# Kernel optimization log

Measured on AMD Instinct MI355X. Metric: run time of the kernel, lower is better.

## Reference

```python
import jax, jax.numpy as jnp
import numpy as np

B, C, M, N = 16, 512, 256, 4096

def setup_inputs() -> dict:
    key = jax.random.key(0)
    k1, k2, k3 = jax.random.split(key, 3)
    x = jax.random.normal(k1, (B, C, N), dtype=jnp.float32)
    # Conv1d(C, M, 1, bias=False) weight: [M, C] (kernel size 1 squeezed)
    Wk = jax.random.normal(k2, (M, C), dtype=jnp.float32) * (1.0 / np.sqrt(C))
    # Conv1d(M, C, 1, bias=False) weight: [C, M]
    Wv = jax.random.normal(k3, (C, M), dtype=jnp.float32) * (1.0 / np.sqrt(M))
    return {"x": x, "Wk": Wk, "Wv": Wv}

def reference(x, Wk, Wv):
    # attn = M_k(x): 1x1 conv == matmul over channel dim -> [B, M, N]
    attn = jnp.einsum("mc,bcn->bmn", Wk, x)
    # softmax over sequence dim N
    attn = jax.nn.softmax(attn, axis=2)
    # L1 normalization over memory-unit (channel) dim M
    attn = attn / (1e-9 + attn.sum(axis=1, keepdims=True))
    # out = M_v(attn): [B, C, N]
    out = jnp.einsum("cm,bmn->bcn", Wv, attn)
    return x + out
```

## Files before the change

kernel.cpp:

```cpp
#include <hip/hip_runtime.h>
#include <hip/hip_bf16.h>

#define Bdim 16
#define Cdim 512
#define Mdim 256
#define Ndim 4096

typedef short bf16x8 __attribute__((ext_vector_type(8)));
typedef float f32x4 __attribute__((ext_vector_type(4)));
typedef unsigned short us8 __attribute__((ext_vector_type(8)));
typedef unsigned short us4 __attribute__((ext_vector_type(4)));

__device__ __forceinline__ unsigned short f2b(float f) {
  union { float f; unsigned int u; } v; v.f = f;
  return (unsigned short)((v.u + 0x8000u) >> 16);
}
__device__ __forceinline__ float b2f(unsigned short h) {
  union { unsigned int u; float f; } v; v.u = ((unsigned int)h) << 16;
  return v.f;
}

__global__ __launch_bounds__(256) void k0_convert(
    const float* __restrict__ gWk, const float* __restrict__ gWv,
    unsigned short* __restrict__ oWk, unsigned short* __restrict__ oWv) {
  const int i = (blockIdx.x * 256 + threadIdx.x) * 4;
  f32x4 a = *reinterpret_cast<const f32x4*>(gWk + i);
  f32x4 b = *reinterpret_cast<const f32x4*>(gWv + i);
  us4 ha, hb;
#pragma unroll
  for (int j = 0; j < 4; ++j) { ha[j] = f2b(a[j]); hb[j] = f2b(b[j]); }
  *reinterpret_cast<us4*>(oWk + i) = ha;
  *reinterpret_cast<us4*>(oWv + i) = hb;
}

#define K1_XPAD 72

__global__ __launch_bounds__(256) void k1_gemm1(
    const float* __restrict__ gx, const unsigned short* __restrict__ gWkB,
    unsigned short* __restrict__ gS) {
  __shared__ unsigned short Wk_s[128 * 64];
  __shared__ unsigned short xT_s[128 * K1_XPAD];
  const int t = threadIdx.x;
  const int b = blockIdx.z;
  const int m0 = blockIdx.y * 128;
  const int n0 = blockIdx.x * 128;
  const int w = t >> 6;
  const int lane = t & 63;
  const int lr = lane & 15;
  const int lg = lane >> 4;
  const int wm = (w >> 1) * 64;
  const int wn = (w & 1) * 64;

  f32x4 acc[4][4] = {};
  const float* xb = gx + (size_t)b * Cdim * Ndim + n0;

  const int snl = t & 63;
  const int scb = (t >> 6) * 16;

  for (int ck = 0; ck < Cdim; ck += 64) {
    {
      const unsigned short* gsrc =
          gWkB + (size_t)(m0 + w * 32 + (lane >> 3)) * Cdim + ck + (lane & 7) * 8;
#pragma unroll
      for (int j = 0; j < 4; ++j) {
        __builtin_amdgcn_global_load_lds(
            (const __attribute__((address_space(1))) unsigned int*)(gsrc + (size_t)j * 8 * Cdim),
            (__attribute__((address_space(3))) unsigned int*)&Wk_s[(w * 32 + j * 8) * 64],
            16, 0, 0);
      }
    }
#pragma unroll
    for (int h = 0; h < 2; ++h) {
      const int n = snl + h * 64;
      const float* src = xb + (size_t)(ck + scb) * Ndim + n;
      float xv[16];
#pragma unroll
      for (int j = 0; j < 16; ++j) xv[j] = src[(size_t)j * Ndim];
      us8 h0, h1;
#pragma unroll
      for (int j = 0; j < 8; ++j) {
        h0[j] = (unsigned short)(__float_as_uint(xv[j]) >> 16);
        h1[j] = (unsigned short)(__float_as_uint(xv[8 + j]) >> 16);
      }
      *reinterpret_cast<us8*>(&xT_s[n * K1_XPAD + scb]) = h0;
      *reinterpret_cast<us8*>(&xT_s[n * K1_XPAD + scb + 8]) = h1;
    }
    __syncthreads();
#pragma unroll
    for (int kk = 0; kk < 64; kk += 32) {
      bf16x8 af[4], bfr[4];
#pragma unroll
      for (int mi = 0; mi < 4; ++mi)
        af[mi] = *reinterpret_cast<const bf16x8*>(
            &Wk_s[(wm + mi * 16 + lr) * 64 + kk + lg * 8]);
#pragma unroll
      for (int ni = 0; ni < 4; ++ni)
        bfr[ni] = *reinterpret_cast<const bf16x8*>(
            &xT_s[(wn + ni * 16 + lr) * K1_XPAD + kk + lg * 8]);
#pragma unroll
      for (int mi = 0; mi < 4; ++mi)
#pragma unroll
        for (int ni = 0; ni < 4; ++ni)
          acc[mi][ni] = __builtin_amdgcn_mfma_f32_16x16x32_bf16(
              af[mi], bfr[ni], acc[mi][ni], 0, 0, 0);
    }
    __syncthreads();
  }
  unsigned short* Sb = gS + ((size_t)b * Mdim + m0 + wm) * Ndim + n0 + wn;
#pragma unroll
  for (int mi = 0; mi < 4; ++mi)
#pragma unroll
    for (int ni = 0; ni < 4; ++ni)
#pragma unroll
      for (int r = 0; r < 4; ++r) {
        int m = mi * 16 + lg * 4 + r;
        int n = ni * 16 + lr;
        Sb[(size_t)m * Ndim + n] = f2b(acc[mi][ni][r]);
      }
}

__global__ __launch_bounds__(256) void k2_rowstats(
    const unsigned short* __restrict__ gS, float2* __restrict__ stats) {
  const int m = blockIdx.x;
  const int b = blockIdx.y;
  const unsigned short* row = gS + ((size_t)b * Mdim + m) * Ndim;
  const int t = threadIdx.x;
  const int w = t >> 6;
  float v[16];
#pragma unroll
  for (int i = 0; i < 2; ++i) {
    us8 u = *reinterpret_cast<const us8*>(row + i * 2048 + t * 8);
#pragma unroll
    for (int j = 0; j < 8; ++j) v[i * 8 + j] = b2f(u[j]);
  }
  float mx = -1e30f;
#pragma unroll
  for (int i = 0; i < 16; ++i) mx = fmaxf(mx, v[i]);
#pragma unroll
  for (int o = 32; o > 0; o >>= 1) mx = fmaxf(mx, __shfl_xor(mx, o, 64));
  __shared__ float redmax[4], redsum[4];
  if ((t & 63) == 0) redmax[w] = mx;
  __syncthreads();
  mx = fmaxf(fmaxf(redmax[0], redmax[1]), fmaxf(redmax[2], redmax[3]));
  float s = 0.f;
#pragma unroll
  for (int i = 0; i < 16; ++i) s += __expf(v[i] - mx);
#pragma unroll
  for (int o = 32; o > 0; o >>= 1) s += __shfl_xor(s, o, 64);
  if ((t & 63) == 0) redsum[w] = s;
  __syncthreads();
  if (t == 0) {
    float tot = redsum[0] + redsum[1] + redsum[2] + redsum[3];
    stats[(size_t)b * Mdim + m] = make_float2(mx, 1.0f / tot);
  }
}

#define K3_PAD 264

__global__ __launch_bounds__(256) void k3_norm(
    const unsigned short* __restrict__ gS, const float2* __restrict__ stats,
    unsigned short* __restrict__ gPT) {
  __shared__ unsigned short P_s[64 * K3_PAD];
  __shared__ float cs[4][64];
  __shared__ float rtot[64];
  const int b = blockIdx.y;
  const int n0 = blockIdx.x * 64;
  const int t = threadIdx.x;
  const int w = t >> 6;
  const int l = t & 63;
  const unsigned short* Sb = gS + ((size_t)b * Mdim + w * 64) * Ndim + n0 + l;
  const float2* stb = stats + (size_t)b * Mdim + w * 64;
  float acc = 0.f;
#pragma unroll
  for (int i8 = 0; i8 < 8; ++i8) {
    us8 pk;
#pragma unroll
    for (int jj = 0; jj < 8; ++jj) {
      const int mi = i8 * 8 + jj;
      float2 st = stb[mi];
      float p = __expf(b2f(Sb[(size_t)mi * Ndim]) - st.x) * st.y;
      acc += p;
      pk[jj] = f2b(p);
    }
    *reinterpret_cast<us8*>(&P_s[l * K3_PAD + w * 64 + i8 * 8]) = pk;
  }
  cs[w][l] = acc;
  __syncthreads();
  if (w == 0) rtot[l] = 1.0f / (1e-9f + cs[0][l] + cs[1][l] + cs[2][l] + cs[3][l]);
  __syncthreads();
  const int mo = (t & 31) * 8;
#pragma unroll
  for (int j = 0; j < 8; ++j) {
    const int n = (t >> 5) + j * 8;
    const float rc = rtot[n];
    us8 pv = *reinterpret_cast<const us8*>(&P_s[n * K3_PAD + mo]);
    us8 o;
#pragma unroll
    for (int q = 0; q < 8; ++q) o[q] = f2b(b2f(pv[q]) * rc);
    *reinterpret_cast<us8*>(gPT + ((size_t)b * Ndim + n0 + n) * Mdim + mo) = o;
  }
}

__global__ __launch_bounds__(256) void k4_gemm2(
    const float* __restrict__ gx, const unsigned short* __restrict__ gWvB,
    const unsigned short* __restrict__ gPT, float* __restrict__ gout) {
  __shared__ unsigned short PT_s[2][128 * 128];
  const int t = threadIdx.x;
  const int b = blockIdx.z;
  const int c0 = blockIdx.y * 128;
  const int n0 = blockIdx.x * 128;
  const int w = t >> 6;
  const int lane = t & 63;
  const int lr = lane & 15;
  const int lg = lane >> 4;
  const int wc = (w >> 1) * 64;
  const int wn = (w & 1) * 64;

  f32x4 acc[4][4] = {};

  {
    const int mo16 = (t & 15) * 16;
    const int r0 = t >> 4;
#pragma unroll
    for (int s = 0; s < 2; ++s) {
      char* tile = reinterpret_cast<char*>(PT_s[s]);
#pragma unroll
      for (int j = 0; j < 8; ++j) {
        const int n = r0 + j * 16;
        us8 v = *reinterpret_cast<const us8*>(
            reinterpret_cast<const char*>(gPT) +
            ((size_t)b * Ndim + n0 + n) * (Mdim * 2) + s * 256 + mo16);
        *reinterpret_cast<us8*>(tile + n * 256 + (mo16 ^ ((n & 7) << 4))) = v;
      }
    }
  }
  __syncthreads();
#pragma unroll
  for (int s = 0; s < 2; ++s) {
    const unsigned short* WvRow = gWvB + (size_t)(c0 + wc + lr) * Mdim + s * 128 + lg * 8;
    const char* tile = reinterpret_cast<const char*>(PT_s[s]);
#pragma unroll
    for (int kk = 0; kk < 128; kk += 32) {
      bf16x8 af[4], bfr[4];
#pragma unroll
      for (int ci = 0; ci < 4; ++ci)
        af[ci] = *reinterpret_cast<const bf16x8*>(WvRow + (size_t)ci * 16 * Mdim + kk);
#pragma unroll
      for (int ni = 0; ni < 4; ++ni) {
        const int rn = wn + ni * 16 + lr;
        bfr[ni] = *reinterpret_cast<const bf16x8*>(
            tile + ((rn * 256 + (kk + lg * 8) * 2) ^ ((rn & 7) << 4)));
      }
#pragma unroll
      for (int ci = 0; ci < 4; ++ci)
#pragma unroll
        for (int ni = 0; ni < 4; ++ni)
          acc[ci][ni] = __builtin_amdgcn_mfma_f32_16x16x32_bf16(
              af[ci], bfr[ni], acc[ci][ni], 0, 0, 0);
    }
  }
  const size_t base = ((size_t)b * Cdim + c0 + wc) * Ndim + n0 + wn;
#pragma unroll
  for (int ci = 0; ci < 4; ++ci)
#pragma unroll
    for (int ni = 0; ni < 4; ++ni)
#pragma unroll
      for (int r = 0; r < 4; ++r) {
        size_t idx = base + (size_t)(ci * 16 + lg * 4 + r) * Ndim + ni * 16 + lr;
        gout[idx] = gx[idx] + acc[ci][ni][r];
      }
}

extern "C" void kernel_launch(void* const* d_in, const int* in_sizes, int n_in,
                              void* d_out, int out_size, void* d_ws, size_t ws_size,
                              hipStream_t stream) {
  const float* x = (const float*)d_in[0];
  const float* Wk = (const float*)d_in[1];
  const float* Wv = (const float*)d_in[2];
  float* out = (float*)d_out;

  unsigned short* S = (unsigned short*)d_ws;
  unsigned short* PT = S + (size_t)Bdim * Mdim * Ndim;
  float2* stats = (float2*)(PT + (size_t)Bdim * Ndim * Mdim);
  unsigned short* WkB = (unsigned short*)(stats + Bdim * Mdim);
  unsigned short* WvB = WkB + Mdim * Cdim;

  k0_convert<<<dim3((Mdim * Cdim) / 1024), 256, 0, stream>>>(Wk, Wv, WkB, WvB);
  k1_gemm1<<<dim3(Ndim / 128, Mdim / 128, Bdim), 256, 0, stream>>>(x, WkB, S);
  k2_rowstats<<<dim3(Mdim, Bdim), 256, 0, stream>>>(S, stats);
  k3_norm<<<dim3(Ndim / 64, Bdim), 256, 0, stream>>>(S, stats, PT);
  k4_gemm2<<<dim3(Ndim / 128, Cdim / 128, Bdim), 256, 0, stream>>>(x, WvB, PT, out);
}
```

Baseline: 143.0 us.

## Swizzle Wk LDS tile and stage Wv/PT via direct global-to-LDS loads

In the first GEMM, the Wk tile loaded into LDS is XOR-swizzled by row so the MFMA fragment reads avoid LDS bank conflicts. In the second GEMM, Wv was previously read straight from global memory for every fragment. It is now staged into LDS together with the PT tile using global_load_lds, with matching swizzles, and processed in two K-halves separated by barriers. This removes repeated uncached-pattern global reads and register round-trips, but adds extra synchronisation and less overlap, since each half must land before compute starts.

```diff
diff --git a/kernel.cpp b/kernel.cpp
--- a/kernel.cpp
+++ b/kernel.cpp
@@ -56,11 +56,13 @@
 
   const int snl = t & 63;
   const int scb = (t >> 6) * 16;
+  const int wrow = lane >> 3;
+  const int wchk = (lane & 7) ^ (wrow & 7);
 
   for (int ck = 0; ck < Cdim; ck += 64) {
     {
       const unsigned short* gsrc =
-          gWkB + (size_t)(m0 + w * 32 + (lane >> 3)) * Cdim + ck + (lane & 7) * 8;
+          gWkB + (size_t)(m0 + w * 32 + wrow) * Cdim + ck + wchk * 8;
 #pragma unroll
       for (int j = 0; j < 4; ++j) {
         __builtin_amdgcn_global_load_lds(
@@ -90,9 +92,12 @@
     for (int kk = 0; kk < 64; kk += 32) {
       bf16x8 af[4], bfr[4];
 #pragma unroll
-      for (int mi = 0; mi < 4; ++mi)
+      for (int mi = 0; mi < 4; ++mi) {
+        const int rm = wm + mi * 16 + lr;
         af[mi] = *reinterpret_cast<const bf16x8*>(
-            &Wk_s[(wm + mi * 16 + lr) * 64 + kk + lg * 8]);
+            reinterpret_cast<const char*>(Wk_s) +
+            rm * 128 + ((kk * 2 + lg * 16) ^ ((rm & 7) << 4)));
+      }
 #pragma unroll
       for (int ni = 0; ni < 4; ++ni)
         bfr[ni] = *reinterpret_cast<const bf16x8*>(
@@ -204,7 +209,8 @@
 __global__ __launch_bounds__(256) void k4_gemm2(
     const float* __restrict__ gx, const unsigned short* __restrict__ gWvB,
     const unsigned short* __restrict__ gPT, float* __restrict__ gout) {
-  __shared__ unsigned short PT_s[2][128 * 128];
+  __shared__ unsigned short Wv_s[128 * 128];
+  __shared__ unsigned short PT_s[128 * 128];
   const int t = threadIdx.x;
   const int b = blockIdx.z;
   const int c0 = blockIdx.y * 128;
@@ -218,38 +224,41 @@
 
   f32x4 acc[4][4] = {};
 
-  {
-    const int mo16 = (t & 15) * 16;
-    const int r0 = t >> 4;
-#pragma unroll
-    for (int s = 0; s < 2; ++s) {
-      char* tile = reinterpret_cast<char*>(PT_s[s]);
-#pragma unroll
-      for (int j = 0; j < 8; ++j) {
-        const int n = r0 + j * 16;
-        us8 v = *reinterpret_cast<const us8*>(
-            reinterpret_cast<const char*>(gPT) +
-            ((size_t)b * Ndim + n0 + n) * (Mdim * 2) + s * 256 + mo16);
-        *reinterpret_cast<us8*>(tile + n * 256 + (mo16 ^ ((n & 7) << 4))) = v;
-      }
-    }
-  }
-  __syncthreads();
-#pragma unroll
+  const int srow = lane >> 4;
+
   for (int s = 0; s < 2; ++s) {
-    const unsigned short* WvRow = gWvB + (size_t)(c0 + wc + lr) * Mdim + s * 128 + lg * 8;
-    const char* tile = reinterpret_cast<const char*>(PT_s[s]);
+#pragma unroll
+    for (int j = 0; j < 8; ++j) {
+      const int r = w * 32 + j * 4 + srow;
+      const int chk = (lane & 15) ^ (r & 7);
+      __builtin_amdgcn_global_load_lds(
+          (const __attribute__((address_space(1))) unsigned int*)(
+              gWvB + (size_t)(c0 + r) * Mdim + s * 128 + chk * 8),
+          (__attribute__((address_space(3))) unsigned int*)&Wv_s[(w * 32 + j * 4) * 128],
+          16, 0, 0);
+      __builtin_amdgcn_global_load_lds(
+          (const __attribute__((address_space(1))) unsigned int*)(
+              gPT + ((size_t)b * Ndim + n0 + r) * Mdim + s * 128 + chk * 8),
+          (__attribute__((address_space(3))) unsigned int*)&PT_s[(w * 32 + j * 4) * 128],
+          16, 0, 0);
+    }
+    __syncthreads();
 #pragma unroll
     for (int kk = 0; kk < 128; kk += 32) {
       bf16x8 af[4], bfr[4];
 #pragma unroll
-      for (int ci = 0; ci < 4; ++ci)
-        af[ci] = *reinterpret_cast<const bf16x8*>(WvRow + (size_t)ci * 16 * Mdim + kk);
+      for (int ci = 0; ci < 4; ++ci) {
+        const int rc = wc + ci * 16 + lr;
+        af[ci] = *reinterpret_cast<const bf16x8*>(
+            reinterpret_cast<const char*>(Wv_s) +
+            rc * 256 + ((kk * 2 + lg * 16) ^ ((rc & 7) << 4)));
+      }
 #pragma unroll
       for (int ni = 0; ni < 4; ++ni) {
         const int rn = wn + ni * 16 + lr;
         bfr[ni] = *reinterpret_cast<const bf16x8*>(
-            tile + ((rn * 256 + (kk + lg * 8) * 2) ^ ((rn & 7) << 4)));
+            reinterpret_cast<const char*>(PT_s) +
+            rn * 256 + ((kk * 2 + lg * 16) ^ ((rn & 7) << 4)));
       }
 #pragma unroll
       for (int ci = 0; ci < 4; ++ci)
@@ -258,6 +267,7 @@
           acc[ci][ni] = __builtin_amdgcn_mfma_f32_16x16x32_bf16(
               af[ci], bfr[ni], acc[ci][ni], 0, 0, 0);
     }
+    __syncthreads();
   }
   const size_t base = ((size_t)b * Cdim + c0 + wc) * Ndim + n0 + wn;
 #pragma unroll
```

Result: faster. 130.8 us (-8.5%).
